# Kernel optimization log

Hardware: AMD Instinct MI355X
Metric: run time of the kernel (lower is better)

## Reference

```python
import jax, jax.numpy as jnp
import numpy as np

N = 16384      # nodes
D_IN = 512     # input_dim
D_OUT = 512    # latent_dim
AVG_DEG = 32.0


def setup_inputs() -> dict:
    key = jax.random.key(0)
    k1, k2, k3, k4 = jax.random.split(key, 4)
    # sparse-ish binary adjacency, stored dense (the torch module densifies anyway)
    p = AVG_DEG / N
    adjacency = (jax.random.uniform(k1, (N, N)) < p).astype(jnp.float32)
    adjacency = jnp.maximum(adjacency, adjacency.T)  # symmetric, no self-loops
    # degree including the self-loop added by the layer (A + I)
    node_degree = jnp.sum(adjacency, axis=1, keepdims=True) + 1.0  # [N,1]
    x = jax.random.normal(k2, (N, D_IN), dtype=jnp.float32)
    W = jax.random.normal(k3, (D_IN, D_OUT), dtype=jnp.float32) * (1.0 / np.sqrt(D_IN))
    b = jax.random.normal(k4, (D_OUT,), dtype=jnp.float32) * 0.01
    return {"x": x, "adjacency": adjacency, "node_degree": node_degree, "W": W, "b": b}


def reference(x, adjacency, node_degree, W, b):
    n = adjacency.shape[0]
    a_hat = adjacency + jnp.eye(n, dtype=adjacency.dtype)      # A + I
    dinv = jax.lax.rsqrt(node_degree)                          # [N,1]
    # faithful torch broadcast: rsqrt(d).mul(A_hat).mul(rsqrt(d)) with [N,1] degree
    a_norm = dinv * a_hat * dinv                               # row-wise D^{-1} scaling
    pooled = a_norm @ x + x                                    # spmm aggregation + residual
    return jax.nn.relu(pooled @ W + b)                         # linear + relu (dropout=0)
```

## Files before the change

### kernel.cpp

```cpp
#include <hip/hip_runtime.h>
#include <hip/hip_bf16.h>

#define NN 16384
#define DD 512
#define CAP 256

typedef __attribute__((ext_vector_type(8))) short bf16x8;
typedef __attribute__((ext_vector_type(4))) float f32x4;
typedef __attribute__((ext_vector_type(4))) float f32x4v;

__global__ __launch_bounds__(256) void wt_kernel(const float* __restrict__ W,
                                                 __hip_bfloat16* __restrict__ WT) {
    __shared__ float tile[32][33];
    const int kb = blockIdx.x * 32;
    const int nb = blockIdx.y * 32;
    const int tx = threadIdx.x;
    const int ty = threadIdx.y;
#pragma unroll
    for (int i = ty; i < 32; i += 8)
        tile[i][tx] = W[(size_t)(kb + i) * DD + nb + tx];
    __syncthreads();
#pragma unroll
    for (int i = ty; i < 32; i += 8)
        WT[(size_t)(nb + i) * DD + kb + tx] = __float2bfloat16(tile[tx][i]);
}

__global__ __launch_bounds__(256) void xb_kernel(const float* __restrict__ x,
                                                 __hip_bfloat16* __restrict__ xb) {
    const size_t p = ((size_t)blockIdx.x * 256 + threadIdx.x) * 4;
    const float4 v = *(const float4*)(x + p);
    union { ushort4 u; __hip_bfloat16 h[4]; } o;
    o.h[0] = __float2bfloat16(v.x);
    o.h[1] = __float2bfloat16(v.y);
    o.h[2] = __float2bfloat16(v.z);
    o.h[3] = __float2bfloat16(v.w);
    *(ushort4*)(xb + p) = o.u;
}

__global__ __launch_bounds__(256) void aggregate_kernel(
        const float* __restrict__ x,
        const __hip_bfloat16* __restrict__ xb,
        const float* __restrict__ adj,
        const float* __restrict__ deg,
        __hip_bfloat16* __restrict__ pooled) {
    __shared__ int cnt;
    __shared__ unsigned short idx[CAP];

    const int i = blockIdx.x;
    const int tid = threadIdx.x;
    if (tid == 0) cnt = 0;
    __syncthreads();

    const f32x4v* row = (const f32x4v*)(adj + (size_t)i * NN);
#pragma unroll
    for (int it = 0; it < NN / (256 * 4); ++it) {
        const int p = tid + it * 256;
        const f32x4v v = __builtin_nontemporal_load(row + p);
        const int c = p * 4;
        if (v.x != 0.f) { int q = atomicAdd(&cnt, 1); if (q < CAP) idx[q] = (unsigned short)(c + 0); }
        if (v.y != 0.f) { int q = atomicAdd(&cnt, 1); if (q < CAP) idx[q] = (unsigned short)(c + 1); }
        if (v.z != 0.f) { int q = atomicAdd(&cnt, 1); if (q < CAP) idx[q] = (unsigned short)(c + 2); }
        if (v.w != 0.f) { int q = atomicAdd(&cnt, 1); if (q < CAP) idx[q] = (unsigned short)(c + 3); }
    }
    __syncthreads();

    const int n = min(cnt, CAP);
    const unsigned* xb32 = (const unsigned*)xb;
    float a0 = 0.f, a1 = 0.f;
    int k = 0;
    for (; k + 8 <= n; k += 8) {
        unsigned v0 = xb32[(size_t)idx[k + 0] * 256 + tid];
        unsigned v1 = xb32[(size_t)idx[k + 1] * 256 + tid];
        unsigned v2 = xb32[(size_t)idx[k + 2] * 256 + tid];
        unsigned v3 = xb32[(size_t)idx[k + 3] * 256 + tid];
        unsigned v4 = xb32[(size_t)idx[k + 4] * 256 + tid];
        unsigned v5 = xb32[(size_t)idx[k + 5] * 256 + tid];
        unsigned v6 = xb32[(size_t)idx[k + 6] * 256 + tid];
        unsigned v7 = xb32[(size_t)idx[k + 7] * 256 + tid];
        a0 += __uint_as_float(v0 << 16); a1 += __uint_as_float(v0 & 0xFFFF0000u);
        a0 += __uint_as_float(v1 << 16); a1 += __uint_as_float(v1 & 0xFFFF0000u);
        a0 += __uint_as_float(v2 << 16); a1 += __uint_as_float(v2 & 0xFFFF0000u);
        a0 += __uint_as_float(v3 << 16); a1 += __uint_as_float(v3 & 0xFFFF0000u);
        a0 += __uint_as_float(v4 << 16); a1 += __uint_as_float(v4 & 0xFFFF0000u);
        a0 += __uint_as_float(v5 << 16); a1 += __uint_as_float(v5 & 0xFFFF0000u);
        a0 += __uint_as_float(v6 << 16); a1 += __uint_as_float(v6 & 0xFFFF0000u);
        a0 += __uint_as_float(v7 << 16); a1 += __uint_as_float(v7 & 0xFFFF0000u);
    }
    for (; k < n; ++k) {
        unsigned v = xb32[(size_t)idx[k] * 256 + tid];
        a0 += __uint_as_float(v << 16); a1 += __uint_as_float(v & 0xFFFF0000u);
    }

    const int d0 = tid * 2;
    const float2 xi = *(const float2*)(x + (size_t)i * DD + d0);
    const float inv = 1.0f / deg[i];
    const float p0 = (a0 + xi.x) * inv + xi.x;
    const float p1 = (a1 + xi.y) * inv + xi.y;
    __hip_bfloat162 h2;
    h2.x = __float2bfloat16(p0);
    h2.y = __float2bfloat16(p1);
    *reinterpret_cast<__hip_bfloat162*>(pooled + (size_t)i * DD + d0) = h2;
}

#define BM 128
#define BN 128
#define BK 64
#define LDT 72

__global__ __launch_bounds__(256) void gemm_bias_relu_kernel(
        const __hip_bfloat16* __restrict__ A,
        const __hip_bfloat16* __restrict__ Bt,
        const float* __restrict__ bias,
        float* __restrict__ out) {
    __shared__ unsigned short As[BM * LDT];
    __shared__ unsigned short Bs[BN * LDT];
    const int tid = threadIdx.x;
    const int wave = tid >> 6, lane = tid & 63;
    const int wr = wave >> 1, wc = wave & 1;
    const int bm = blockIdx.y * BM, bn = blockIdx.x * BN;
    const int lr = lane & 15, kg = lane >> 4;
    const int sr = tid >> 3;
    const int ss = tid & 7;

    f32x4 acc[4][4] = {};

    for (int kk = 0; kk < DD; kk += BK) {
        __syncthreads();
#pragma unroll
        for (int it = 0; it < 4; ++it) {
            const int r = sr + it * 32;
            *(int4*)&As[r * LDT + ss * 8] = *(const int4*)(A + (size_t)(bm + r) * DD + kk + ss * 8);
            *(int4*)&Bs[r * LDT + ss * 8] = *(const int4*)(Bt + (size_t)(bn + r) * DD + kk + ss * 8);
        }
        __syncthreads();
#pragma unroll
        for (int ki = 0; ki < BK; ki += 32) {
            bf16x8 a[4], b[4];
#pragma unroll
            for (int m = 0; m < 4; ++m)
                a[m] = *(const bf16x8*)&As[(wr * 64 + m * 16 + lr) * LDT + ki + kg * 8];
#pragma unroll
            for (int n2 = 0; n2 < 4; ++n2)
                b[n2] = *(const bf16x8*)&Bs[(wc * 64 + n2 * 16 + lr) * LDT + ki + kg * 8];
#pragma unroll
            for (int m = 0; m < 4; ++m)
#pragma unroll
                for (int n2 = 0; n2 < 4; ++n2)
                    acc[m][n2] = __builtin_amdgcn_mfma_f32_16x16x32_bf16(a[m], b[n2], acc[m][n2], 0, 0, 0);
        }
    }

#pragma unroll
    for (int m = 0; m < 4; ++m) {
        const int row = bm + wr * 64 + m * 16 + kg * 4;
#pragma unroll
        for (int n2 = 0; n2 < 4; ++n2) {
            const int col = bn + wc * 64 + n2 * 16 + lr;
            const float bv = bias[col];
#pragma unroll
            for (int r = 0; r < 4; ++r) {
                float v = acc[m][n2][r] + bv;
                out[(size_t)(row + r) * DD + col] = v > 0.f ? v : 0.f;
            }
        }
    }
}

extern "C" void kernel_launch(void* const* d_in, const int* in_sizes, int n_in,
                              void* d_out, int out_size, void* d_ws, size_t ws_size,
                              hipStream_t stream) {
    (void)in_sizes; (void)n_in; (void)out_size; (void)ws_size;
    const float* x   = (const float*)d_in[0];
    const float* adj = (const float*)d_in[1];
    const float* deg = (const float*)d_in[2];
    const float* W   = (const float*)d_in[3];
    const float* b   = (const float*)d_in[4];
    float* out = (float*)d_out;

    __hip_bfloat16* pooled = (__hip_bfloat16*)d_ws;
    __hip_bfloat16* WT     = pooled + (size_t)NN * DD;
    __hip_bfloat16* xb     = WT + (size_t)DD * DD;

    xb_kernel<<<NN * DD / (256 * 4), 256, 0, stream>>>(x, xb);
    wt_kernel<<<dim3(DD / 32, DD / 32), dim3(32, 8), 0, stream>>>(W, WT);
    aggregate_kernel<<<NN, 256, 0, stream>>>(x, xb, adj, deg, pooled);
    gemm_bias_relu_kernel<<<dim3(DD / BN, NN / BM), 256, 0, stream>>>(pooled, WT, b, out);
}
```

Baseline: 1.455 ms.

## Process one adjacency row per wavefront with ballot compaction instead of LDS atomics

The aggregate kernel now gives each wavefront its own adjacency row, four rows per block. Nonzero column indices are compacted with wave ballot and popcount rather than shared-memory atomics, which also removes the block barriers. The gather phase has each lane load 8 bf16 values (16 bytes) per neighbor row and keeps 8 accumulators. The kernel is still bound by streaming the dense 1 GB adjacency, so most of the benefit depends on how much the atomics and barriers were limiting that scan.

```diff
diff --git a/kernel.cpp b/kernel.cpp
--- a/kernel.cpp
+++ b/kernel.cpp
@@ -7,7 +7,7 @@
 
 typedef __attribute__((ext_vector_type(8))) short bf16x8;
 typedef __attribute__((ext_vector_type(4))) float f32x4;
-typedef __attribute__((ext_vector_type(4))) float f32x4v;
+typedef __attribute__((ext_vector_type(4))) unsigned int u32x4;
 
 __global__ __launch_bounds__(256) void wt_kernel(const float* __restrict__ W,
                                                  __hip_bfloat16* __restrict__ WT) {
@@ -43,63 +43,110 @@
         const float* __restrict__ adj,
         const float* __restrict__ deg,
         __hip_bfloat16* __restrict__ pooled) {
-    __shared__ int cnt;
-    __shared__ unsigned short idx[CAP];
-
-    const int i = blockIdx.x;
-    const int tid = threadIdx.x;
-    if (tid == 0) cnt = 0;
-    __syncthreads();
-
-    const f32x4v* row = (const f32x4v*)(adj + (size_t)i * NN);
-#pragma unroll
-    for (int it = 0; it < NN / (256 * 4); ++it) {
-        const int p = tid + it * 256;
-        const f32x4v v = __builtin_nontemporal_load(row + p);
-        const int c = p * 4;
-        if (v.x != 0.f) { int q = atomicAdd(&cnt, 1); if (q < CAP) idx[q] = (unsigned short)(c + 0); }
-        if (v.y != 0.f) { int q = atomicAdd(&cnt, 1); if (q < CAP) idx[q] = (unsigned short)(c + 1); }
-        if (v.z != 0.f) { int q = atomicAdd(&cnt, 1); if (q < CAP) idx[q] = (unsigned short)(c + 2); }
-        if (v.w != 0.f) { int q = atomicAdd(&cnt, 1); if (q < CAP) idx[q] = (unsigned short)(c + 3); }
-    }
-    __syncthreads();
-
+    __shared__ unsigned short sidx[4][CAP];
+
+    const int tid  = threadIdx.x;
+    const int w    = tid >> 6;
+    const int lane = tid & 63;
+    const int i    = blockIdx.x * 4 + w;
+
+    const u32x4* row = (const u32x4*)(adj + (size_t)i * NN);
+    const unsigned long long lmask = ((unsigned long long)1 << lane) - 1;
+    int cnt = 0;
+#pragma unroll 4
+    for (int it = 0; it < NN / (64 * 4); ++it) {
+        const u32x4 v = __builtin_nontemporal_load(row + it * 64 + lane);
+        const int cbase = it * 256 + lane * 4;
+        {
+            unsigned long long m = __ballot(v.x != 0u);
+            if (m) {
+                if (v.x != 0u) {
+                    int pos = cnt + (int)__popcll(m & lmask);
+                    if (pos < CAP) sidx[w][pos] = (unsigned short)(cbase + 0);
+                }
+                cnt += (int)__popcll(m);
+            }
+        }
+        {
+            unsigned long long m = __ballot(v.y != 0u);
+            if (m) {
+                if (v.y != 0u) {
+                    int pos = cnt + (int)__popcll(m & lmask);
+                    if (pos < CAP) sidx[w][pos] = (unsigned short)(cbase + 1);
+                }
+                cnt += (int)__popcll(m);
+            }
+        }
+        {
+            unsigned long long m = __ballot(v.z != 0u);
+            if (m) {
+                if (v.z != 0u) {
+                    int pos = cnt + (int)__popcll(m & lmask);
+                    if (pos < CAP) sidx[w][pos] = (unsigned short)(cbase + 2);
+                }
+                cnt += (int)__popcll(m);
+            }
+        }
+        {
+            unsigned long long m = __ballot(v.w != 0u);
+            if (m) {
+                if (v.w != 0u) {
+                    int pos = cnt + (int)__popcll(m & lmask);
+                    if (pos < CAP) sidx[w][pos] = (unsigned short)(cbase + 3);
+                }
+                cnt += (int)__popcll(m);
+            }
+        }
+    }
     const int n = min(cnt, CAP);
-    const unsigned* xb32 = (const unsigned*)xb;
-    float a0 = 0.f, a1 = 0.f;
+
+    float a0 = 0.f, a1 = 0.f, a2 = 0.f, a3 = 0.f;
+    float a4 = 0.f, a5 = 0.f, a6 = 0.f, a7 = 0.f;
+    const unsigned* xbrow;
+#define ACC_ROW(J)                                                          \
+    do {                                                                    \
+        xbrow = (const unsigned*)(xb + (size_t)(J) * DD + lane * 8);        \
+        const uint4 u = *(const uint4*)xbrow;                               \
+        a0 += __uint_as_float(u.x << 16); a1 += __uint_as_float(u.x & 0xFFFF0000u); \
+        a2 += __uint_as_float(u.y << 16); a3 += __uint_as_float(u.y & 0xFFFF0000u); \
+        a4 += __uint_as_float(u.z << 16); a5 += __uint_as_float(u.z & 0xFFFF0000u); \
+        a6 += __uint_as_float(u.w << 16); a7 += __uint_as_float(u.w & 0xFFFF0000u); \
+    } while (0)
+
     int k = 0;
-    for (; k + 8 <= n; k += 8) {
-        unsigned v0 = xb32[(size_t)idx[k + 0] * 256 + tid];
-        unsigned v1 = xb32[(size_t)idx[k + 1] * 256 + tid];
-        unsigned v2 = xb32[(size_t)idx[k + 2] * 256 + tid];
-        unsigned v3 = xb32[(size_t)idx[k + 3] * 256 + tid];
-        unsigned v4 = xb32[(size_t)idx[k + 4] * 256 + tid];
-        unsigned v5 = xb32[(size_t)idx[k + 5] * 256 + tid];
-        unsigned v6 = xb32[(size_t)idx[k + 6] * 256 + tid];
-        unsigned v7 = xb32[(size_t)idx[k + 7] * 256 + tid];
-        a0 += __uint_as_float(v0 << 16); a1 += __uint_as_float(v0 & 0xFFFF0000u);
-        a0 += __uint_as_float(v1 << 16); a1 += __uint_as_float(v1 & 0xFFFF0000u);
-        a0 += __uint_as_float(v2 << 16); a1 += __uint_as_float(v2 & 0xFFFF0000u);
-        a0 += __uint_as_float(v3 << 16); a1 += __uint_as_float(v3 & 0xFFFF0000u);
-        a0 += __uint_as_float(v4 << 16); a1 += __uint_as_float(v4 & 0xFFFF0000u);
-        a0 += __uint_as_float(v5 << 16); a1 += __uint_as_float(v5 & 0xFFFF0000u);
-        a0 += __uint_as_float(v6 << 16); a1 += __uint_as_float(v6 & 0xFFFF0000u);
-        a0 += __uint_as_float(v7 << 16); a1 += __uint_as_float(v7 & 0xFFFF0000u);
-    }
-    for (; k < n; ++k) {
-        unsigned v = xb32[(size_t)idx[k] * 256 + tid];
-        a0 += __uint_as_float(v << 16); a1 += __uint_as_float(v & 0xFFFF0000u);
-    }
-
-    const int d0 = tid * 2;
-    const float2 xi = *(const float2*)(x + (size_t)i * DD + d0);
+    for (; k + 4 <= n; k += 4) {
+        const ushort4 jj = *(const ushort4*)&sidx[w][k];
+        ACC_ROW(jj.x);
+        ACC_ROW(jj.y);
+        ACC_ROW(jj.z);
+        ACC_ROW(jj.w);
+    }
+    for (; k < n; ++k) ACC_ROW(sidx[w][k]);
+#undef ACC_ROW
+
+    const float* xi = x + (size_t)i * DD + lane * 8;
+    const float4 x0 = *(const float4*)(xi);
+    const float4 x1 = *(const float4*)(xi + 4);
     const float inv = 1.0f / deg[i];
-    const float p0 = (a0 + xi.x) * inv + xi.x;
-    const float p1 = (a1 + xi.y) * inv + xi.y;
-    __hip_bfloat162 h2;
-    h2.x = __float2bfloat16(p0);
-    h2.y = __float2bfloat16(p1);
-    *reinterpret_cast<__hip_bfloat162*>(pooled + (size_t)i * DD + d0) = h2;
+    float p0 = (a0 + x0.x) * inv + x0.x;
+    float p1 = (a1 + x0.y) * inv + x0.y;
+    float p2 = (a2 + x0.z) * inv + x0.z;
+    float p3 = (a3 + x0.w) * inv + x0.w;
+    float p4 = (a4 + x1.x) * inv + x1.x;
+    float p5 = (a5 + x1.y) * inv + x1.y;
+    float p6 = (a6 + x1.z) * inv + x1.z;
+    float p7 = (a7 + x1.w) * inv + x1.w;
+
+    union { uint4 u; unsigned short h[8]; } o;
+    o.h[0] = __bfloat16_as_ushort(__float2bfloat16(p0));
+    o.h[1] = __bfloat16_as_ushort(__float2bfloat16(p1));
+    o.h[2] = __bfloat16_as_ushort(__float2bfloat16(p2));
+    o.h[3] = __bfloat16_as_ushort(__float2bfloat16(p3));
+    o.h[4] = __bfloat16_as_ushort(__float2bfloat16(p4));
+    o.h[5] = __bfloat16_as_ushort(__float2bfloat16(p5));
+    o.h[6] = __bfloat16_as_ushort(__float2bfloat16(p6));
+    o.h[7] = __bfloat16_as_ushort(__float2bfloat16(p7));
+    *(uint4*)(pooled + (size_t)i * DD + lane * 8) = o.u;
 }
 
 #define BM 128
@@ -183,6 +230,6 @@
 
     xb_kernel<<<NN * DD / (256 * 4), 256, 0, stream>>>(x, xb);
     wt_kernel<<<dim3(DD / 32, DD / 32), dim3(32, 8), 0, stream>>>(W, WT);
-    aggregate_kernel<<<NN, 256, 0, stream>>>(x, xb, adj, deg, pooled);
+    aggregate_kernel<<<NN / 4, 256, 0, stream>>>(x, xb, adj, deg, pooled);
     gemm_bias_relu_kernel<<<dim3(DD / BN, NN / BM), 256, 0, stream>>>(pooled, WT, b, out);
 }
```

Result: no change. 1.427 ms (-1.9%).
